# Kernel tuning notes

Measured on AMD Instinct MI355X. Metric: run time of the kernel, lower is better.

Reference implementation:

```python
import jax, jax.numpy as jnp
import numpy as np

CLASS_EMBED_DIM = 128
TOPK = 64
EPS = float(np.finfo(float).eps)
ALPHA = 0.99


def setup_inputs() -> dict:
    key = jax.random.key(0)
    k1, k2, k3 = jax.random.split(key, 3)
    b, n, d = 16, 256, 640  # d = embed_dim + class_embed_dim
    embed_dim, inner_dim = 512, 512
    x = jax.random.normal(k1, (b, n, d), dtype=jnp.float32)
    # kaiming-normal style init: std = sqrt(2 / fan_in)
    std = (2.0 / embed_dim) ** 0.5
    Wq = jax.random.normal(k2, (embed_dim, inner_dim), dtype=jnp.float32) * std
    Wk = jax.random.normal(k3, (embed_dim, inner_dim), dtype=jnp.float32) * std
    alpha = jnp.float32(ALPHA)
    return {"x": x, "Wq": Wq, "Wk": Wk, "alpha": alpha}


def reference(x, Wq, Wk, alpha):
    b, n, d = x.shape
    xf = x.reshape(b * n, d)            # (N, embed+class)
    xe = xf[:, :-CLASS_EMBED_DIM]       # (N, embed)
    q = xe @ Wq                         # (N, inner)
    k = xe @ Wk                         # (N, inner)
    D = q.shape[1]
    # dots[i,j] = mean_d (q_i - k_j)^2, via expansion (avoids N x N x D tensor)
    q2 = jnp.sum(q * q, axis=1)
    k2 = jnp.sum(k * k, axis=1)
    dots = (q2[:, None] + k2[None, :] - 2.0 * (q @ k.T)) / D  # (N, N)
    N = dots.shape[0]
    _, idx = jax.lax.top_k(dots, TOPK)  # largest, matching torch.topk
    mask = jnp.zeros_like(dots).at[jnp.arange(N)[:, None], idx].set(1.0)
    mask = ((mask + mask.T) > 0).astype(jnp.float32)
    attn = dots * mask
    A = jnp.eye(N, dtype=dots.dtype) - alpha * attn + EPS
    out = jnp.linalg.inv(A) @ xf        # (N, d); to_v is identity
    return out.reshape(b, n, d)
```

## Files before the change

kernel.cpp:

```cpp
#include <hip/hip_runtime.h>
#include <float.h>

#define NN 4096
#define DD 640
#define DE 512
#define NB 16
#define OB 128
#define NOB (NN/OB)
#define SB 128
#define NSB (NN/SB)

static __device__ __forceinline__ float4 ldg4(const float* p) { return *(const float4*)p; }

__global__ __launch_bounds__(256) void proj_gemm(
    const float* __restrict__ xf, const float* __restrict__ Wq,
    const float* __restrict__ Wk, float* __restrict__ q, float* __restrict__ kk_)
{
  __shared__ float Xs[32][68], Qs[32][68], Ks[32][68];
  const int i0 = blockIdx.x * 64, c0 = blockIdx.y * 64;
  const int t = threadIdx.x, tr = t >> 4, tc = t & 15;
  float accq[4][4] = {}, acck[4][4] = {};
  for (int kb = 0; kb < DE; kb += 32) {
    {
      int m = t >> 3, k4 = (t & 7) << 2;
      float4 v0 = ldg4(xf + (size_t)(i0 + m) * DD + kb + k4);
      float4 v1 = ldg4(xf + (size_t)(i0 + m + 32) * DD + kb + k4);
      Xs[k4+0][m] = v0.x; Xs[k4+1][m] = v0.y; Xs[k4+2][m] = v0.z; Xs[k4+3][m] = v0.w;
      Xs[k4+0][m+32] = v1.x; Xs[k4+1][m+32] = v1.y; Xs[k4+2][m+32] = v1.z; Xs[k4+3][m+32] = v1.w;
    }
    {
      int kr = t >> 3, n8 = (t & 7) << 3;
      *(float4*)&Qs[kr][n8]   = ldg4(Wq + (size_t)(kb + kr) * DE + c0 + n8);
      *(float4*)&Qs[kr][n8+4] = ldg4(Wq + (size_t)(kb + kr) * DE + c0 + n8 + 4);
      *(float4*)&Ks[kr][n8]   = ldg4(Wk + (size_t)(kb + kr) * DE + c0 + n8);
      *(float4*)&Ks[kr][n8+4] = ldg4(Wk + (size_t)(kb + kr) * DE + c0 + n8 + 4);
    }
    __syncthreads();
    #pragma unroll
    for (int kkk = 0; kkk < 32; ++kkk) {
      float a[4], bq[4], bk[4];
      *(float4*)a  = *(const float4*)&Xs[kkk][tr << 2];
      *(float4*)bq = *(const float4*)&Qs[kkk][tc << 2];
      *(float4*)bk = *(const float4*)&Ks[kkk][tc << 2];
      #pragma unroll
      for (int r = 0; r < 4; ++r)
        #pragma unroll
        for (int c = 0; c < 4; ++c) { accq[r][c] += a[r]*bq[c]; acck[r][c] += a[r]*bk[c]; }
    }
    __syncthreads();
  }
  #pragma unroll
  for (int r = 0; r < 4; ++r) {
    float* qp = q   + (size_t)(i0 + (tr<<2) + r) * DE + c0 + (tc<<2);
    float* kp = kk_ + (size_t)(i0 + (tr<<2) + r) * DE + c0 + (tc<<2);
    *(float4*)qp = make_float4(accq[r][0], accq[r][1], accq[r][2], accq[r][3]);
    *(float4*)kp = make_float4(acck[r][0], acck[r][1], acck[r][2], acck[r][3]);
  }
}

__global__ __launch_bounds__(256) void rownorm(
    const float* __restrict__ q, const float* __restrict__ kk_,
    float* __restrict__ q2, float* __restrict__ k2)
{
  int w = (blockIdx.x * 256 + threadIdx.x) >> 6;
  int lane = threadIdx.x & 63;
  const float* src = (w < NN) ? q : kk_;
  int row = (w < NN) ? w : w - NN;
  const float* p = src + (size_t)row * DE;
  float s = 0.f;
  for (int c = lane; c < DE; c += 64) { float v = p[c]; s += v * v; }
  for (int off = 32; off; off >>= 1) s += __shfl_down(s, off);
  if (lane == 0) { if (w < NN) q2[row] = s; else k2[row] = s; }
}

__global__ __launch_bounds__(256) void dots_gemm128(
    const float* __restrict__ q, const float* __restrict__ kk_,
    const float* __restrict__ q2, const float* __restrict__ k2,
    float* __restrict__ dots)
{
  __shared__ float As[16][132], Bs[16][132];
  const int i0 = blockIdx.x * 128, j0 = blockIdx.y * 128;
  const int t = threadIdx.x;
  const int tr = t >> 4, tc = t & 15;
  float acc[8][8] = {};
  for (int kb = 0; kb < DE; kb += 16) {
    {
      int m = t >> 1, k8 = (t & 1) << 3;
      const float* ap = q + (size_t)(i0 + m) * DE + kb + k8;
      float4 v0 = ldg4(ap), v1 = ldg4(ap + 4);
      As[k8+0][m] = v0.x; As[k8+1][m] = v0.y; As[k8+2][m] = v0.z; As[k8+3][m] = v0.w;
      As[k8+4][m] = v1.x; As[k8+5][m] = v1.y; As[k8+6][m] = v1.z; As[k8+7][m] = v1.w;
      const float* bp = kk_ + (size_t)(j0 + m) * DE + kb + k8;
      float4 w0 = ldg4(bp), w1 = ldg4(bp + 4);
      Bs[k8+0][m] = w0.x; Bs[k8+1][m] = w0.y; Bs[k8+2][m] = w0.z; Bs[k8+3][m] = w0.w;
      Bs[k8+4][m] = w1.x; Bs[k8+5][m] = w1.y; Bs[k8+6][m] = w1.z; Bs[k8+7][m] = w1.w;
    }
    __syncthreads();
    #pragma unroll
    for (int k = 0; k < 16; ++k) {
      float av[8], bv[8];
      *(float4*)av       = *(const float4*)&As[k][tr << 3];
      *(float4*)(av + 4) = *(const float4*)&As[k][(tr << 3) + 4];
      *(float4*)bv       = *(const float4*)&Bs[k][tc << 3];
      *(float4*)(bv + 4) = *(const float4*)&Bs[k][(tc << 3) + 4];
      #pragma unroll
      for (int r = 0; r < 8; ++r)
        #pragma unroll
        for (int c = 0; c < 8; ++c) acc[r][c] += av[r] * bv[c];
    }
    __syncthreads();
  }
  const float inv = 1.0f / (float)DE;
  float k2v[8];
  *(float4*)k2v       = ldg4(k2 + j0 + (tc << 3));
  *(float4*)(k2v + 4) = ldg4(k2 + j0 + (tc << 3) + 4);
  #pragma unroll
  for (int r = 0; r < 8; ++r) {
    float q2v = q2[i0 + (tr << 3) + r];
    float o[8];
    #pragma unroll
    for (int c = 0; c < 8; ++c) o[c] = (q2v + k2v[c] - 2.0f * acc[r][c]) * inv;
    float* dp = dots + (size_t)(i0 + (tr << 3) + r) * NN + j0 + (tc << 3);
    *(float4*)dp       = make_float4(o[0], o[1], o[2], o[3]);
    *(float4*)(dp + 4) = make_float4(o[4], o[5], o[6], o[7]);
  }
}

__global__ __launch_bounds__(256) void topk_bits(
    const float* __restrict__ dots, unsigned int* __restrict__ bits)
{
  __shared__ float row[NN];
  __shared__ unsigned int b[128];
  __shared__ float rv[4]; __shared__ int ri[4];
  const int i = blockIdx.x, t = threadIdx.x;
  const float* dr = dots + (size_t)i * NN;
  for (int c = t; c < NN; c += 256) row[c] = dr[c];
  if (t < 128) b[t] = 0u;
  __syncthreads();
  for (int it = 0; it < 64; ++it) {
    float bv = -FLT_MAX; int bi = NN;
    for (int c = t; c < NN; c += 256) { float v = row[c]; if (v > bv) { bv = v; bi = c; } }
    for (int off = 32; off; off >>= 1) {
      float ov = __shfl_down(bv, off); int oi = __shfl_down(bi, off);
      if (ov > bv || (ov == bv && oi < bi)) { bv = ov; bi = oi; }
    }
    if ((t & 63) == 0) { rv[t >> 6] = bv; ri[t >> 6] = bi; }
    __syncthreads();
    if (t == 0) {
      float fv = rv[0]; int fi = ri[0];
      for (int w = 1; w < 4; ++w)
        if (rv[w] > fv || (rv[w] == fv && ri[w] < fi)) { fv = rv[w]; fi = ri[w]; }
      b[fi >> 5] |= 1u << (fi & 31);
      row[fi] = -FLT_MAX;
    }
    __syncthreads();
  }
  if (t < 128) bits[(size_t)i * 128 + t] = b[t];
}

__global__ __launch_bounds__(256) void build_A(
    float* __restrict__ A, const unsigned int* __restrict__ bits,
    const float* __restrict__ alpha_p)
{
  int tid = blockIdx.x * 256 + threadIdx.x;
  int i = tid >> 10;
  int j4 = (tid & 1023) << 2;
  float alpha = alpha_p[0];
  float* p = A + (size_t)i * NN + j4;
  float4 d = *(float4*)p;
  unsigned int wrow = bits[(size_t)i * 128 + (j4 >> 5)];
  float dv[4] = {d.x, d.y, d.z, d.w}, o[4];
  #pragma unroll
  for (int u = 0; u < 4; ++u) {
    int j = j4 + u;
    unsigned int m1 = (wrow >> (j & 31)) & 1u;
    unsigned int m2 = (bits[(size_t)j * 128 + (i >> 5)] >> (i & 31)) & 1u;
    float base = (i == j) ? 1.0f : 0.0f;
    o[u] = base - ((m1 | m2) ? alpha * dv[u] : 0.0f);
  }
  *(float4*)p = make_float4(o[0], o[1], o[2], o[3]);
}

__global__ __launch_bounds__(256) void pack_panel(
    const float* __restrict__ A, float* __restrict__ P, int ok0)
{
  int r = blockIdx.x * 8 + (threadIdx.x >> 5);
  int c4 = (threadIdx.x & 31) << 2;
  if (r < NN - ok0)
    *(float4*)(P + (size_t)r * OB + c4) = ldg4(A + (size_t)(ok0 + r) * NN + ok0 + c4);
}

__global__ __launch_bounds__(256) void unpack_panel(
    const float* __restrict__ P, float* __restrict__ A, int ok0)
{
  int r = blockIdx.x * 8 + (threadIdx.x >> 5);
  int c4 = (threadIdx.x & 31) << 2;
  if (r < NN - ok0)
    *(float4*)(A + (size_t)(ok0 + r) * NN + ok0 + c4) = ldg4(P + (size_t)r * OB + c4);
}

__global__ __launch_bounds__(1024) void lu_panel(
    float* __restrict__ P, int k0, int ok0, int* __restrict__ piv)
{
  const int t = threadIdx.x;
  const int M = NN - k0;
  const int lk0 = k0 - ok0;
  float a[4][NB];
  __shared__ float rv[2][16]; __shared__ int ri[2][16];
  __shared__ float pb[2][NB];
  __shared__ float bufA[2][NB];
  __shared__ int piv_s[NB];
  __shared__ int sd[32], ss[32];
  __shared__ float l16[16][17];
  __shared__ float gbuf[32][112];

  #pragma unroll
  for (int i = 0; i < 4; ++i) {
    int r = t + (i << 10);
    if (r < M) {
      const float* src = P + (size_t)(lk0 + r) * OB + lk0;
      #pragma unroll
      for (int c4 = 0; c4 < NB; c4 += 4) {
        float4 v = ldg4(src + c4);
        a[i][c4] = v.x; a[i][c4+1] = v.y; a[i][c4+2] = v.z; a[i][c4+3] = v.w;
      }
    }
  }

  #pragma unroll
  for (int j = 0; j < NB; ++j) {
    const int bb = j & 1;
    float bv = -1.0f; int br = 1 << 30;
    #pragma unroll
    for (int i = 0; i < 4; ++i) {
      int r = t + (i << 10);
      if (r >= j && r < M) {
        float v = fabsf(a[i][j]);
        if (v > bv || (v == bv && r < br)) { bv = v; br = r; }
      }
    }
    for (int off = 32; off; off >>= 1) {
      float ov = __shfl_down(bv, off); int orr = __shfl_down(br, off);
      if (ov > bv || (ov == bv && orr < br)) { bv = ov; br = orr; }
    }
    if ((t & 63) == 0) { rv[bb][t >> 6] = bv; ri[bb][t >> 6] = br; }
    __syncthreads();
    float fv = rv[bb][0]; int fr = ri[bb][0];
    #pragma unroll
    for (int w = 1; w < 16; ++w)
      if (rv[bb][w] > fv || (rv[bb][w] == fv && ri[bb][w] < fr)) { fv = rv[bb][w]; fr = ri[bb][w]; }
    const int pr = fr;
    if (t == 0) piv_s[j] = k0 + pr;
    const int prT = pr & 1023, prS = pr >> 10;
    if (t == prT) {
      #pragma unroll
      for (int i2 = 0; i2 < 4; ++i2) if (i2 == prS) {
        #pragma unroll
        for (int c = 0; c < NB; ++c) pb[bb][c] = a[i2][c];
      }
    }
    if (t == j) {
      #pragma unroll
      for (int c = 0; c < NB; ++c) bufA[bb][c] = a[0][c];
    }
    __syncthreads();
    if (t == j) {
      #pragma unroll
      for (int c = 0; c < NB; ++c) a[0][c] = pb[bb][c];
    }
    if (t == prT) {
      #pragma unroll
      for (int i2 = 0; i2 < 4; ++i2) if (i2 == prS) {
        #pragma unroll
        for (int c = 0; c < NB; ++c) a[i2][c] = bufA[bb][c];
      }
    }
    float rp = 1.0f / pb[bb][j];
    #pragma unroll
    for (int i = 0; i < 4; ++i) {
      int r = t + (i << 10);
      if (r > j && r < M) {
        float mlt = a[i][j] * rp;
        a[i][j] = mlt;
        #pragma unroll
        for (int c = j + 1; c < NB; ++c) a[i][c] -= mlt * pb[bb][c];
      }
    }
  }
  __syncthreads();

  #pragma unroll
  for (int i = 0; i < 4; ++i) {
    int r = t + (i << 10);
    if (r < M) {
      float* dst = P + (size_t)(lk0 + r) * OB + lk0;
      #pragma unroll
      for (int c4 = 0; c4 < NB; c4 += 4)
        *(float4*)(dst + c4) = make_float4(a[i][c4], a[i][c4+1], a[i][c4+2], a[i][c4+3]);
    }
  }
  if (t < NB) piv[k0 + t] = piv_s[t];

  if (t < 16) {
    #pragma unroll
    for (int c2 = 0; c2 < NB; ++c2) l16[t][c2] = a[0][c2];
  }

  if (t < 32) {
    int slotrow = (t < NB) ? (k0 + t) : -1;
    int content = slotrow;
    int next_ext = NB;
    for (int j = 0; j < NB; ++j) {
      int p = piv_s[j];
      unsigned long long mask = __ballot(slotrow == p);
      int bslot;
      if (mask) bslot = __ffsll((unsigned long long)mask) - 1;
      else {
        bslot = next_ext;
        if (t == next_ext) { slotrow = p; content = p; }
        next_ext++;
      }
      int srcl = (t == j) ? bslot : ((t == bslot) ? j : t);
      content = __shfl(content, srcl);
    }
    sd[t] = slotrow;
    ss[t] = content;
  }
  __syncthreads();

  const int p16 = lk0;
  for (int idx = t; idx < 32 * 112; idx += 1024) {
    int i = idx / 112, cc = idx - i * 112;
    if (sd[i] >= 0 && sd[i] != ss[i]) {
      int cl = (cc < p16 ? cc : cc + NB);
      gbuf[i][cc] = P[(size_t)(ss[i] - ok0) * OB + cl];
    }
  }
  __syncthreads();
  for (int idx = t; idx < 32 * 112; idx += 1024) {
    int i = idx / 112, cc = idx - i * 112;
    if (sd[i] >= 0 && sd[i] != ss[i]) {
      int cl = (cc < p16 ? cc : cc + NB);
      P[(size_t)(sd[i] - ok0) * OB + cl] = gbuf[i][cc];
    }
  }
  __syncthreads();

  const int w = OB - (lk0 + NB);
  if (t < w) {
    int cl = lk0 + NB + t;
    int cc = p16 + t;
    float x[16];
    #pragma unroll
    for (int i = 0; i < 16; ++i)
      x[i] = (ss[i] != sd[i]) ? gbuf[i][cc] : P[(size_t)(lk0 + i) * OB + cl];
    #pragma unroll
    for (int i = 1; i < 16; ++i)
      #pragma unroll
      for (int j = 0; j < i; ++j) x[i] -= l16[i][j] * x[j];
    #pragma unroll
    for (int i = 0; i < 16; ++i) P[(size_t)(lk0 + i) * OB + cl] = x[i];
  }
}

__global__ __launch_bounds__(64) void net_perm128(
    const int* __restrict__ piv_g, int ok0,
    int* __restrict__ nd, int* __restrict__ ns)
{
  __shared__ int pl[OB];
  const int L = threadIdx.x;
  pl[L] = piv_g[ok0 + L];
  pl[L + 64] = piv_g[ok0 + 64 + L];
  __syncthreads();
  int c0 = ok0 + L, c1 = ok0 + 64 + L, c2 = -1, c3 = -1;
  int sr2 = -1, sr3 = -1;
  int next_ext = 128;
  for (int j = 0; j < OB; ++j) {
    int p = pl[j];
    int s2;
    if (p < ok0 + OB) s2 = p - ok0;
    else {
      unsigned long long m2 = __ballot(sr2 == p);
      unsigned long long m3 = __ballot(sr3 == p);
      if (m2) s2 = 128 + (__ffsll(m2) - 1);
      else if (m3) s2 = 192 + (__ffsll(m3) - 1);
      else {
        s2 = next_ext;
        if (s2 < 192) { if (L == s2 - 128) { sr2 = p; c2 = p; } }
        else          { if (L == s2 - 192) { sr3 = p; c3 = p; } }
        next_ext++;
      }
    }
    int jp = j >> 6, jl = j & 63, sp = s2 >> 6, sl = s2 & 63;
    int vj0 = __shfl(c0, jl), vj1 = __shfl(c1, jl);
    int vj = (jp == 0) ? vj0 : vj1;
    int vs0 = __shfl(c0, sl), vs1 = __shfl(c1, sl), vs2 = __shfl(c2, sl), vs3 = __shfl(c3, sl);
    int vs = (sp == 0) ? vs0 : (sp == 1) ? vs1 : (sp == 2) ? vs2 : vs3;
    if (jp == 0 && L == jl) c0 = vs;
    if (jp == 1 && L == jl) c1 = vs;
    if (sp == 0 && L == sl) c0 = vj;
    if (sp == 1 && L == sl) c1 = vj;
    if (sp == 2 && L == sl) c2 = vj;
    if (sp == 3 && L == sl) c3 = vj;
  }
  nd[L] = ok0 + L;        ns[L] = c0;
  nd[64 + L] = ok0 + 64 + L; ns[64 + L] = c1;
  nd[128 + L] = sr2;      ns[128 + L] = c2;
  nd[192 + L] = sr3;      ns[192 + L] = c3;
}

__global__ __launch_bounds__(256) void perm_copy_out(
    const float* __restrict__ A, float* __restrict__ T,
    const int* __restrict__ nd, const int* __restrict__ ns, int ok0)
{
  int s = blockIdx.y;
  int d = nd[s], sr = ns[s];
  if (d < 0 || d == sr) return;
  int c = blockIdx.x * 1024 + threadIdx.x * 4;
  if (c >= ok0 && c < ok0 + OB) return;
  *(float4*)(T + (size_t)s * NN + c) = ldg4(A + (size_t)sr * NN + c);
}

__global__ __launch_bounds__(256) void perm_copy_in(
    float* __restrict__ A, const float* __restrict__ T,
    const int* __restrict__ nd, const int* __restrict__ ns, int ok0)
{
  int s = blockIdx.y;
  int d = nd[s], sr = ns[s];
  if (d < 0 || d == sr) return;
  int c = blockIdx.x * 1024 + threadIdx.x * 4;
  if (c >= ok0 && c < ok0 + OB) return;
  *(float4*)(A + (size_t)d * NN + c) = ldg4(T + (size_t)s * NN + c);
}

__global__ __launch_bounds__(64) void trsm128L(float* __restrict__ A, int ok0)
{
  __shared__ float Ls[64][65];
  __shared__ float xs[64][133];
  const int t = threadIdx.x;
  const int c = ok0 + OB + blockIdx.x * 64 + t;
  for (int i = 0; i < 128; ++i) xs[t][i] = A[(size_t)(ok0 + i) * NN + c];
  for (int i = 0; i < 64; ++i) Ls[i][t] = A[(size_t)(ok0 + i) * NN + ok0 + t];
  __syncthreads();
  for (int i = 1; i < 64; ++i) {
    float s0 = 0.f, s1 = 0.f, s2 = 0.f, s3 = 0.f;
    int j = 0;
    for (; j + 3 < i; j += 4) {
      s0 += Ls[i][j+0] * xs[t][j+0]; s1 += Ls[i][j+1] * xs[t][j+1];
      s2 += Ls[i][j+2] * xs[t][j+2]; s3 += Ls[i][j+3] * xs[t][j+3];
    }
    for (; j < i; ++j) s0 += Ls[i][j] * xs[t][j];
    xs[t][i] -= (s0 + s1) + (s2 + s3);
  }
  __syncthreads();
  for (int i = 0; i < 64; ++i) Ls[i][t] = A[(size_t)(ok0 + 64 + i) * NN + ok0 + t];
  __syncthreads();
  for (int i = 0; i < 64; ++i) {
    float s0 = 0.f, s1 = 0.f, s2 = 0.f, s3 = 0.f;
    #pragma unroll 4
    for (int j = 0; j < 64; j += 4) {
      s0 += Ls[i][j+0] * xs[t][j+0]; s1 += Ls[i][j+1] * xs[t][j+1];
      s2 += Ls[i][j+2] * xs[t][j+2]; s3 += Ls[i][j+3] * xs[t][j+3];
    }
    xs[t][64 + i] -= (s0 + s1) + (s2 + s3);
  }
  __syncthreads();
  for (int i = 0; i < 64; ++i) Ls[i][t] = A[(size_t)(ok0 + 64 + i) * NN + ok0 + 64 + t];
  __syncthreads();
  for (int i = 1; i < 64; ++i) {
    float s0 = 0.f, s1 = 0.f, s2 = 0.f, s3 = 0.f;
    int j = 0;
    for (; j + 3 < i; j += 4) {
      s0 += Ls[i][j+0] * xs[t][64+j+0]; s1 += Ls[i][j+1] * xs[t][64+j+1];
      s2 += Ls[i][j+2] * xs[t][64+j+2]; s3 += Ls[i][j+3] * xs[t][64+j+3];
    }
    for (; j < i; ++j) s0 += Ls[i][j] * xs[t][64+j];
    xs[t][64 + i] -= (s0 + s1) + (s2 + s3);
  }
  for (int i = 0; i < 128; ++i) A[(size_t)(ok0 + i) * NN + c] = xs[t][i];
}

__global__ __launch_bounds__(256) void rank_update(
    float* __restrict__ C, int ldc,
    const float* __restrict__ Aop, int lda,
    const float* __restrict__ Bop, int ldb,
    int Mr, int Nc, int K)
{
  __shared__ float As[16][68], Bs[16][68];
  const int m0 = blockIdx.x * 64, n0 = blockIdx.y * 64;
  const int t = threadIdx.x, tr = t >> 4, tc = t & 15;
  const float4 z4 = make_float4(0.f, 0.f, 0.f, 0.f);
  float acc[4][4] = {};
  for (int kb = 0; kb < K; kb += 16) {
    {
      int m = t >> 2, k4 = (t & 3) << 2;
      float4 v0 = (m0 + m < Mr) ? ldg4(Aop + (size_t)(m0 + m) * lda + kb + k4) : z4;
      As[k4+0][m] = v0.x; As[k4+1][m] = v0.y; As[k4+2][m] = v0.z; As[k4+3][m] = v0.w;
    }
    {
      int kr = t >> 4, n4 = (t & 15) << 2;
      bool ok = (n0 + n4 < Nc);
      float4 w0 = ok ? ldg4(Bop + (size_t)(kb + kr) * ldb + n0 + n4) : z4;
      *(float4*)&Bs[kr][n4] = w0;
    }
    __syncthreads();
    #pragma unroll
    for (int kkk = 0; kkk < 16; ++kkk) {
      float a[4], b[4];
      *(float4*)a = *(const float4*)&As[kkk][tr << 2];
      *(float4*)b = *(const float4*)&Bs[kkk][tc << 2];
      #pragma unroll
      for (int r = 0; r < 4; ++r)
        #pragma unroll
        for (int c = 0; c < 4; ++c) acc[r][c] += a[r] * b[c];
    }
    __syncthreads();
  }
  #pragma unroll
  for (int r = 0; r < 4; ++r) {
    int m = m0 + (tr << 2) + r;
    int n = n0 + (tc << 2);
    if (m < Mr && n < Nc) {
      float* cp = C + (size_t)m * ldc + n;
      float4 cv = *(float4*)cp;
      cv.x -= acc[r][0]; cv.y -= acc[r][1]; cv.z -= acc[r][2]; cv.w -= acc[r][3];
      *(float4*)cp = cv;
    }
  }
}

__global__ __launch_bounds__(256) void rank_update128(
    float* __restrict__ C, int ldc,
    const float* __restrict__ Aop, int lda,
    const float* __restrict__ Bop, int ldb,
    int K)
{
  __shared__ float As[16][132], Bs[16][132];
  const int m0 = blockIdx.x * 128, n0 = blockIdx.y * 128;
  const int t = threadIdx.x;
  const int tr = t >> 4, tc = t & 15;
  float acc[8][8] = {};
  for (int kb = 0; kb < K; kb += 16) {
    {
      int m = t >> 1, k8 = (t & 1) << 3;
      const float* ap = Aop + (size_t)(m0 + m) * lda + kb + k8;
      float4 v0 = ldg4(ap), v1 = ldg4(ap + 4);
      As[k8+0][m] = v0.x; As[k8+1][m] = v0.y; As[k8+2][m] = v0.z; As[k8+3][m] = v0.w;
      As[k8+4][m] = v1.x; As[k8+5][m] = v1.y; As[k8+6][m] = v1.z; As[k8+7][m] = v1.w;
    }
    {
      int kr = t >> 4, c8 = (t & 15) << 3;
      const float* bp = Bop + (size_t)(kb + kr) * ldb + n0 + c8;
      *(float4*)&Bs[kr][c8]     = ldg4(bp);
      *(float4*)&Bs[kr][c8 + 4] = ldg4(bp + 4);
    }
    __syncthreads();
    #pragma unroll
    for (int k = 0; k < 16; ++k) {
      float av[8], bv[8];
      *(float4*)av       = *(const float4*)&As[k][tr << 3];
      *(float4*)(av + 4) = *(const float4*)&As[k][(tr << 3) + 4];
      *(float4*)bv       = *(const float4*)&Bs[k][tc << 3];
      *(float4*)(bv + 4) = *(const float4*)&Bs[k][(tc << 3) + 4];
      #pragma unroll
      for (int r = 0; r < 8; ++r)
        #pragma unroll
        for (int c = 0; c < 8; ++c) acc[r][c] += av[r] * bv[c];
    }
    __syncthreads();
  }
  #pragma unroll
  for (int r = 0; r < 8; ++r) {
    float* cp = C + (size_t)(m0 + (tr << 3) + r) * ldc + n0 + (tc << 3);
    float4 c0 = *(float4*)cp, c1 = *(float4*)(cp + 4);
    c0.x -= acc[r][0]; c0.y -= acc[r][1]; c0.z -= acc[r][2]; c0.w -= acc[r][3];
    c1.x -= acc[r][4]; c1.y -= acc[r][5]; c1.z -= acc[r][6]; c1.w -= acc[r][7];
    *(float4*)cp = c0; *(float4*)(cp + 4) = c1;
  }
}

__global__ __launch_bounds__(128) void inv_tri(
    const float* __restrict__ Ag, float* __restrict__ invT, int upper)
{
  __shared__ float xs[128][128];
  const int s = blockIdx.x, t = threadIdx.x;
  const size_t r0 = (size_t)s * SB;
  for (int i = 0; i < 128; ++i) xs[i][t] = 0.0f;
  const float* Tb = Ag + r0 * NN + r0;
  if (!upper) {
    xs[t][t] = 1.0f;
    for (int i = 1; i < 128; ++i) {
      float s0 = 0.f, s1 = 0.f, s2 = 0.f, s3 = 0.f;
      int j = 0;
      for (; j + 3 < i; j += 4) {
        s0 += Tb[(size_t)i * NN + j+0] * xs[j+0][t];
        s1 += Tb[(size_t)i * NN + j+1] * xs[j+1][t];
        s2 += Tb[(size_t)i * NN + j+2] * xs[j+2][t];
        s3 += Tb[(size_t)i * NN + j+3] * xs[j+3][t];
      }
      for (; j < i; ++j) s0 += Tb[(size_t)i * NN + j] * xs[j][t];
      float ssum = (s0 + s1) + (s2 + s3);
      if (i != t) xs[i][t] = -ssum;
    }
  } else {
    xs[t][t] = 1.0f / Tb[(size_t)t * NN + t];
    for (int i = 126; i >= 0; --i) {
      float s0 = 0.f, s1 = 0.f, s2 = 0.f, s3 = 0.f;
      int j = i + 1;
      for (; j + 3 < 128; j += 4) {
        s0 += Tb[(size_t)i * NN + j+0] * xs[j+0][t];
        s1 += Tb[(size_t)i * NN + j+1] * xs[j+1][t];
        s2 += Tb[(size_t)i * NN + j+2] * xs[j+2][t];
        s3 += Tb[(size_t)i * NN + j+3] * xs[j+3][t];
      }
      for (; j < 128; ++j) s0 += Tb[(size_t)i * NN + j] * xs[j][t];
      float ssum = (s0 + s1) + (s2 + s3);
      if (i != t) xs[i][t] = -ssum / Tb[(size_t)i * NN + i];
    }
  }
  for (int i = 0; i < 128; ++i) invT[(size_t)s * SB * SB + (size_t)i * SB + t] = xs[i][t];
}

__global__ __launch_bounds__(1024) void perm_compose(
    const int* __restrict__ piv, int* __restrict__ idxp)
{
  __shared__ int pl[NN];
  const int t = threadIdx.x;
  for (int j = t; j < NN; j += 1024) pl[j] = piv[j];
  __syncthreads();
  int pos[4] = { t, t + 1024, t + 2048, t + 3072 };
  for (int j = NN - 1; j >= 0; --j) {
    int p = pl[j];
    #pragma unroll
    for (int u = 0; u < 4; ++u) {
      int r = t + (u << 10);
      if (j <= r) {
        if (pos[u] == j) pos[u] = p;
        else if (pos[u] == p) pos[u] = j;
      }
    }
  }
  #pragma unroll
  for (int u = 0; u < 4; ++u) idxp[t + (u << 10)] = pos[u];
}

__global__ __launch_bounds__(256) void gather_rows(
    const float* __restrict__ xf, const int* __restrict__ idxp, float* __restrict__ out)
{
  const int r = blockIdx.x, t = threadIdx.x;
  const int src = idxp[r];
  const float4* s = (const float4*)(xf + (size_t)src * DD);
  float4* d = (float4*)(out + (size_t)r * DD);
  for (int c = t; c < DD / 4; c += 256) d[c] = s[c];
}

__global__ __launch_bounds__(256) void diag_apply(
    float* __restrict__ B, const float* __restrict__ Minv, int r0)
{
  __shared__ float Bs[128][68];
  const int c0 = blockIdx.x * 64, t = threadIdx.x;
  #pragma unroll
  for (int v = 0; v < 8; ++v) {
    int id = t + v * 256;
    int k = id >> 4, c4 = (id & 15) << 2;
    *(float4*)&Bs[k][c4] = ldg4(B + (size_t)(r0 + k) * DD + c0 + c4);
  }
  __syncthreads();
  const int tr = t >> 4, tc = t & 15;
  float acc[8][4] = {};
  for (int k4 = 0; k4 < 128; k4 += 4) {
    float b0[4], b1[4], b2[4], b3[4];
    *(float4*)b0 = *(const float4*)&Bs[k4+0][tc << 2];
    *(float4*)b1 = *(const float4*)&Bs[k4+1][tc << 2];
    *(float4*)b2 = *(const float4*)&Bs[k4+2][tc << 2];
    *(float4*)b3 = *(const float4*)&Bs[k4+3][tc << 2];
    #pragma unroll
    for (int rr = 0; rr < 8; ++rr) {
      float m[4]; *(float4*)m = ldg4(Minv + (size_t)(tr*8 + rr) * SB + k4);
      #pragma unroll
      for (int c = 0; c < 4; ++c)
        acc[rr][c] += m[0]*b0[c] + m[1]*b1[c] + m[2]*b2[c] + m[3]*b3[c];
    }
  }
  #pragma unroll
  for (int rr = 0; rr < 8; ++rr)
    *(float4*)(B + (size_t)(r0 + tr*8 + rr) * DD + c0 + (tc << 2)) =
        make_float4(acc[rr][0], acc[rr][1], acc[rr][2], acc[rr][3]);
}

extern "C" void kernel_launch(void* const* d_in, const int* in_sizes, int n_in,
                              void* d_out, int out_size, void* d_ws, size_t ws_size,
                              hipStream_t stream)
{
  const float* xf    = (const float*)d_in[0];
  const float* Wq    = (const float*)d_in[1];
  const float* Wk    = (const float*)d_in[2];
  const float* alpha = (const float*)d_in[3];
  float* out = (float*)d_out;
  char* ws = (char*)d_ws;

  float* Amat = (float*)(ws);
  float* q    = (float*)(ws + 67108864ull);
  float* kbuf = (float*)(ws + 75497472ull);
  float* invL = (float*)(ws + 83886080ull);
  float* invU = (float*)(ws + 85983232ull);
  unsigned int* bits = (unsigned int*)(ws + 88080384ull);
  float* q2   = (float*)(ws + 90177536ull);
  float* k2   = (float*)(ws + 90193920ull);
  int* piv    = (int*)(ws + 90210304ull);
  int* idxp   = (int*)(ws + 90226688ull);
  int* nd     = (int*)(ws + 90243072ull);
  int* ns     = (int*)(ws + 90275840ull);
  float* Tbuf = q;
  float* P    = kbuf;

  proj_gemm<<<dim3(NN/64, DE/64), 256, 0, stream>>>(xf, Wq, Wk, q, kbuf);
  rownorm<<<2 * NN / 4, 256, 0, stream>>>(q, kbuf, q2, k2);
  dots_gemm128<<<dim3(NN/128, NN/128), 256, 0, stream>>>(q, kbuf, q2, k2, Amat);
  topk_bits<<<NN, 256, 0, stream>>>(Amat, bits);
  build_A<<<NN * NN / 4 / 256, 256, 0, stream>>>(Amat, bits, alpha);

  for (int ob = 0; ob < NOB; ++ob) {
    const int ok0 = ob * OB;
    const int nrows = NN - ok0;
    pack_panel<<<(nrows + 7) / 8, 256, 0, stream>>>(Amat, P, ok0);
    for (int p = 0; p < OB / NB; ++p) {
      const int k0 = ok0 + p * NB;
      lu_panel<<<1, 1024, 0, stream>>>(P, k0, ok0, piv);
      if (p < OB / NB - 1) {
        const int lk1 = (p + 1) * NB;
        const int w = OB - lk1;
        const int M2 = nrows - lk1;
        rank_update<<<dim3((M2 + 63) / 64, (w + 63) / 64), 256, 0, stream>>>(
            P + (size_t)lk1 * OB + lk1, OB,
            P + (size_t)lk1 * OB + (lk1 - NB), OB,
            P + (size_t)(lk1 - NB) * OB + lk1, OB,
            M2, w, NB);
      }
    }
    unpack_panel<<<(nrows + 7) / 8, 256, 0, stream>>>(P, Amat, ok0);
    net_perm128<<<1, 64, 0, stream>>>(piv, ok0, nd, ns);
    perm_copy_out<<<dim3(NN / 1024, 256), 256, 0, stream>>>(Amat, Tbuf, nd, ns, ok0);
    perm_copy_in<<<dim3(NN / 1024, 256), 256, 0, stream>>>(Amat, Tbuf, nd, ns, ok0);
    const int b1 = ok0 + OB;
    const int M2 = NN - b1;
    if (M2 > 0) {
      trsm128L<<<M2 / 64, 64, 0, stream>>>(Amat, ok0);
      rank_update128<<<dim3(M2 / 128, M2 / 128), 256, 0, stream>>>(
          Amat + (size_t)b1 * NN + b1, NN,
          Amat + (size_t)b1 * NN + ok0, NN,
          Amat + (size_t)ok0 * NN + b1, NN,
          OB);
    }
  }

  inv_tri<<<NSB, 128, 0, stream>>>(Amat, invL, 0);
  inv_tri<<<NSB, 128, 0, stream>>>(Amat, invU, 1);
  perm_compose<<<1, 1024, 0, stream>>>(piv, idxp);
  gather_rows<<<NN, 256, 0, stream>>>(xf, idxp, out);

  for (int s = 0; s < NSB; ++s) {
    int r0 = s * SB;
    diag_apply<<<DD / 64, 256, 0, stream>>>(out, invL + (size_t)s * SB * SB, r0);
    if (r0 + SB < NN) {
      int M2 = NN - r0 - SB;
      rank_update128<<<dim3(M2 / 128, DD / 128), 256, 0, stream>>>(
          out + (size_t)(r0 + SB) * DD, DD,
          Amat + (size_t)(r0 + SB) * NN + r0, NN,
          out + (size_t)r0 * DD, DD,
          SB);
    }
  }
  for (int s = NSB - 1; s >= 0; --s) {
    int r0 = s * SB;
    diag_apply<<<DD / 64, 256, 0, stream>>>(out, invU + (size_t)s * SB * SB, r0);
    if (r0 > 0) {
      rank_update128<<<dim3(r0 / 128, DD / 128), 256, 0, stream>>>(
          out, DD,
          Amat + r0, NN,
          out + (size_t)r0 * DD, DD,
          SB);
    }
  }
}
```

Before: 39.65 ms.

## Fuse panel LU and rank updates into one cooperative kernel with grid sync

Replaces the per-16-column sequence of lu_panel and rank_update launches with a single cooperative kernel per 128-wide block column. Workgroup 0 factors each sub-panel and the whole grid of 120 workgroups then does the trailing update, with grid.sync between phases. The goal is to remove about 15 kernel launches per outer block and the gaps between them. In exchange the factoring block drops from 1024 to 512 threads with more registers per thread, and each step pays for grid-wide barriers.

```diff
diff --git a/kernel.cpp b/kernel.cpp
--- a/kernel.cpp
+++ b/kernel.cpp
@@ -1,5 +1,8 @@
 #include <hip/hip_runtime.h>
+#include <hip/hip_cooperative_groups.h>
 #include <float.h>
+
+namespace cg = cooperative_groups;
 
 #define NN 4096
 #define DD 640
@@ -9,6 +12,7 @@
 #define NOB (NN/OB)
 #define SB 128
 #define NSB (NN/SB)
+#define LU_NWG 120
 
 static __device__ __forceinline__ float4 ldg4(const float* p) { return *(const float4*)p; }
 
@@ -199,167 +203,230 @@
     *(float4*)(A + (size_t)(ok0 + r) * NN + ok0 + c4) = ldg4(P + (size_t)r * OB + c4);
 }
 
-__global__ __launch_bounds__(1024) void lu_panel(
-    float* __restrict__ P, int k0, int ok0, int* __restrict__ piv)
-{
+__global__ __launch_bounds__(512) void lu_block_coop(
+    float* __restrict__ P, int ok0, int* __restrict__ piv)
+{
+  cg::grid_group grid = cg::this_grid();
   const int t = threadIdx.x;
-  const int M = NN - k0;
-  const int lk0 = k0 - ok0;
-  float a[4][NB];
-  __shared__ float rv[2][16]; __shared__ int ri[2][16];
+  const int wg = blockIdx.x;
+  const int nwg = gridDim.x;
+  const int nrows = NN - ok0;
+
+  __shared__ float rv[2][8]; __shared__ int ri[2][8];
   __shared__ float pb[2][NB];
   __shared__ float bufA[2][NB];
   __shared__ int piv_s[NB];
   __shared__ int sd[32], ss[32];
   __shared__ float l16[16][17];
   __shared__ float gbuf[32][112];
-
-  #pragma unroll
-  for (int i = 0; i < 4; ++i) {
-    int r = t + (i << 10);
-    if (r < M) {
-      const float* src = P + (size_t)(lk0 + r) * OB + lk0;
+  __shared__ float As[16][68], Bs[16][68];
+
+  for (int p = 0; p < OB / NB; ++p) {
+    const int k0 = ok0 + p * NB;
+    const int lk0 = p * NB;
+    const int M = NN - k0;
+
+    if (wg == 0) {
+      float a[8][NB];
       #pragma unroll
-      for (int c4 = 0; c4 < NB; c4 += 4) {
-        float4 v = ldg4(src + c4);
-        a[i][c4] = v.x; a[i][c4+1] = v.y; a[i][c4+2] = v.z; a[i][c4+3] = v.w;
-      }
-    }
-  }
-
-  #pragma unroll
-  for (int j = 0; j < NB; ++j) {
-    const int bb = j & 1;
-    float bv = -1.0f; int br = 1 << 30;
-    #pragma unroll
-    for (int i = 0; i < 4; ++i) {
-      int r = t + (i << 10);
-      if (r >= j && r < M) {
-        float v = fabsf(a[i][j]);
-        if (v > bv || (v == bv && r < br)) { bv = v; br = r; }
-      }
-    }
-    for (int off = 32; off; off >>= 1) {
-      float ov = __shfl_down(bv, off); int orr = __shfl_down(br, off);
-      if (ov > bv || (ov == bv && orr < br)) { bv = ov; br = orr; }
-    }
-    if ((t & 63) == 0) { rv[bb][t >> 6] = bv; ri[bb][t >> 6] = br; }
-    __syncthreads();
-    float fv = rv[bb][0]; int fr = ri[bb][0];
-    #pragma unroll
-    for (int w = 1; w < 16; ++w)
-      if (rv[bb][w] > fv || (rv[bb][w] == fv && ri[bb][w] < fr)) { fv = rv[bb][w]; fr = ri[bb][w]; }
-    const int pr = fr;
-    if (t == 0) piv_s[j] = k0 + pr;
-    const int prT = pr & 1023, prS = pr >> 10;
-    if (t == prT) {
+      for (int i = 0; i < 8; ++i) {
+        int r = t + (i << 9);
+        if (r < M) {
+          const float* src = P + (size_t)(lk0 + r) * OB + lk0;
+          #pragma unroll
+          for (int c4 = 0; c4 < NB; c4 += 4) {
+            float4 v = ldg4(src + c4);
+            a[i][c4] = v.x; a[i][c4+1] = v.y; a[i][c4+2] = v.z; a[i][c4+3] = v.w;
+          }
+        }
+      }
       #pragma unroll
-      for (int i2 = 0; i2 < 4; ++i2) if (i2 == prS) {
-        #pragma unroll
-        for (int c = 0; c < NB; ++c) pb[bb][c] = a[i2][c];
-      }
-    }
-    if (t == j) {
+      for (int j = 0; j < NB; ++j) {
+        const int bb = j & 1;
+        float bv = -1.0f; int br = 1 << 30;
+        #pragma unroll
+        for (int i = 0; i < 8; ++i) {
+          int r = t + (i << 9);
+          if (r >= j && r < M) {
+            float v = fabsf(a[i][j]);
+            if (v > bv || (v == bv && r < br)) { bv = v; br = r; }
+          }
+        }
+        for (int off = 32; off; off >>= 1) {
+          float ov = __shfl_down(bv, off); int orr = __shfl_down(br, off);
+          if (ov > bv || (ov == bv && orr < br)) { bv = ov; br = orr; }
+        }
+        if ((t & 63) == 0) { rv[bb][t >> 6] = bv; ri[bb][t >> 6] = br; }
+        __syncthreads();
+        float fv = rv[bb][0]; int fr = ri[bb][0];
+        #pragma unroll
+        for (int w = 1; w < 8; ++w)
+          if (rv[bb][w] > fv || (rv[bb][w] == fv && ri[bb][w] < fr)) { fv = rv[bb][w]; fr = ri[bb][w]; }
+        const int pr = fr;
+        if (t == 0) piv_s[j] = k0 + pr;
+        const int prT = pr & 511, prS = pr >> 9;
+        if (t == prT) {
+          #pragma unroll
+          for (int i2 = 0; i2 < 8; ++i2) if (i2 == prS) {
+            #pragma unroll
+            for (int c = 0; c < NB; ++c) pb[bb][c] = a[i2][c];
+          }
+        }
+        if (t == j) {
+          #pragma unroll
+          for (int c = 0; c < NB; ++c) bufA[bb][c] = a[0][c];
+        }
+        __syncthreads();
+        if (t == j) {
+          #pragma unroll
+          for (int c = 0; c < NB; ++c) a[0][c] = pb[bb][c];
+        }
+        if (t == prT) {
+          #pragma unroll
+          for (int i2 = 0; i2 < 8; ++i2) if (i2 == prS) {
+            #pragma unroll
+            for (int c = 0; c < NB; ++c) a[i2][c] = bufA[bb][c];
+          }
+        }
+        float rp = 1.0f / pb[bb][j];
+        #pragma unroll
+        for (int i = 0; i < 8; ++i) {
+          int r = t + (i << 9);
+          if (r > j && r < M) {
+            float mlt = a[i][j] * rp;
+            a[i][j] = mlt;
+            #pragma unroll
+            for (int c = j + 1; c < NB; ++c) a[i][c] -= mlt * pb[bb][c];
+          }
+        }
+      }
+      __syncthreads();
+
       #pragma unroll
-      for (int c = 0; c < NB; ++c) bufA[bb][c] = a[0][c];
-    }
-    __syncthreads();
-    if (t == j) {
-      #pragma unroll
-      for (int c = 0; c < NB; ++c) a[0][c] = pb[bb][c];
-    }
-    if (t == prT) {
-      #pragma unroll
-      for (int i2 = 0; i2 < 4; ++i2) if (i2 == prS) {
-        #pragma unroll
-        for (int c = 0; c < NB; ++c) a[i2][c] = bufA[bb][c];
-      }
-    }
-    float rp = 1.0f / pb[bb][j];
-    #pragma unroll
-    for (int i = 0; i < 4; ++i) {
-      int r = t + (i << 10);
-      if (r > j && r < M) {
-        float mlt = a[i][j] * rp;
-        a[i][j] = mlt;
-        #pragma unroll
-        for (int c = j + 1; c < NB; ++c) a[i][c] -= mlt * pb[bb][c];
-      }
-    }
-  }
-  __syncthreads();
-
-  #pragma unroll
-  for (int i = 0; i < 4; ++i) {
-    int r = t + (i << 10);
-    if (r < M) {
-      float* dst = P + (size_t)(lk0 + r) * OB + lk0;
-      #pragma unroll
-      for (int c4 = 0; c4 < NB; c4 += 4)
-        *(float4*)(dst + c4) = make_float4(a[i][c4], a[i][c4+1], a[i][c4+2], a[i][c4+3]);
-    }
-  }
-  if (t < NB) piv[k0 + t] = piv_s[t];
-
-  if (t < 16) {
-    #pragma unroll
-    for (int c2 = 0; c2 < NB; ++c2) l16[t][c2] = a[0][c2];
-  }
-
-  if (t < 32) {
-    int slotrow = (t < NB) ? (k0 + t) : -1;
-    int content = slotrow;
-    int next_ext = NB;
-    for (int j = 0; j < NB; ++j) {
-      int p = piv_s[j];
-      unsigned long long mask = __ballot(slotrow == p);
-      int bslot;
-      if (mask) bslot = __ffsll((unsigned long long)mask) - 1;
-      else {
-        bslot = next_ext;
-        if (t == next_ext) { slotrow = p; content = p; }
-        next_ext++;
-      }
-      int srcl = (t == j) ? bslot : ((t == bslot) ? j : t);
-      content = __shfl(content, srcl);
-    }
-    sd[t] = slotrow;
-    ss[t] = content;
-  }
-  __syncthreads();
-
-  const int p16 = lk0;
-  for (int idx = t; idx < 32 * 112; idx += 1024) {
-    int i = idx / 112, cc = idx - i * 112;
-    if (sd[i] >= 0 && sd[i] != ss[i]) {
-      int cl = (cc < p16 ? cc : cc + NB);
-      gbuf[i][cc] = P[(size_t)(ss[i] - ok0) * OB + cl];
-    }
-  }
-  __syncthreads();
-  for (int idx = t; idx < 32 * 112; idx += 1024) {
-    int i = idx / 112, cc = idx - i * 112;
-    if (sd[i] >= 0 && sd[i] != ss[i]) {
-      int cl = (cc < p16 ? cc : cc + NB);
-      P[(size_t)(sd[i] - ok0) * OB + cl] = gbuf[i][cc];
-    }
-  }
-  __syncthreads();
-
-  const int w = OB - (lk0 + NB);
-  if (t < w) {
-    int cl = lk0 + NB + t;
-    int cc = p16 + t;
-    float x[16];
-    #pragma unroll
-    for (int i = 0; i < 16; ++i)
-      x[i] = (ss[i] != sd[i]) ? gbuf[i][cc] : P[(size_t)(lk0 + i) * OB + cl];
-    #pragma unroll
-    for (int i = 1; i < 16; ++i)
-      #pragma unroll
-      for (int j = 0; j < i; ++j) x[i] -= l16[i][j] * x[j];
-    #pragma unroll
-    for (int i = 0; i < 16; ++i) P[(size_t)(lk0 + i) * OB + cl] = x[i];
+      for (int i = 0; i < 8; ++i) {
+        int r = t + (i << 9);
+        if (r < M) {
+          float* dst = P + (size_t)(lk0 + r) * OB + lk0;
+          #pragma unroll
+          for (int c4 = 0; c4 < NB; c4 += 4)
+            *(float4*)(dst + c4) = make_float4(a[i][c4], a[i][c4+1], a[i][c4+2], a[i][c4+3]);
+        }
+      }
+      if (t < NB) piv[k0 + t] = piv_s[t];
+
+      if (t < 16) {
+        #pragma unroll
+        for (int c2 = 0; c2 < NB; ++c2) l16[t][c2] = a[0][c2];
+      }
+
+      if (t < 32) {
+        int slotrow = (t < NB) ? (k0 + t) : -1;
+        int content = slotrow;
+        int next_ext = NB;
+        for (int j = 0; j < NB; ++j) {
+          int pp = piv_s[j];
+          unsigned long long mask = __ballot(slotrow == pp);
+          int bslot;
+          if (mask) bslot = __ffsll((unsigned long long)mask) - 1;
+          else {
+            bslot = next_ext;
+            if (t == next_ext) { slotrow = pp; content = pp; }
+            next_ext++;
+          }
+          int srcl = (t == j) ? bslot : ((t == bslot) ? j : t);
+          content = __shfl(content, srcl);
+        }
+        sd[t] = slotrow;
+        ss[t] = content;
+      }
+      __syncthreads();
+
+      const int p16 = lk0;
+      for (int idx = t; idx < 32 * 112; idx += 512) {
+        int i = idx / 112, cc = idx - i * 112;
+        if (sd[i] >= 0 && sd[i] != ss[i]) {
+          int cl = (cc < p16 ? cc : cc + NB);
+          gbuf[i][cc] = P[(size_t)(ss[i] - ok0) * OB + cl];
+        }
+      }
+      __syncthreads();
+      for (int idx = t; idx < 32 * 112; idx += 512) {
+        int i = idx / 112, cc = idx - i * 112;
+        if (sd[i] >= 0 && sd[i] != ss[i]) {
+          int cl = (cc < p16 ? cc : cc + NB);
+          P[(size_t)(sd[i] - ok0) * OB + cl] = gbuf[i][cc];
+        }
+      }
+      __syncthreads();
+
+      const int w = OB - (lk0 + NB);
+      if (t < w) {
+        int cl = lk0 + NB + t;
+        int cc = p16 + t;
+        float x[16];
+        #pragma unroll
+        for (int i = 0; i < 16; ++i)
+          x[i] = (ss[i] != sd[i]) ? gbuf[i][cc] : P[(size_t)(lk0 + i) * OB + cl];
+        #pragma unroll
+        for (int i = 1; i < 16; ++i)
+          #pragma unroll
+          for (int j = 0; j < i; ++j) x[i] -= l16[i][j] * x[j];
+        #pragma unroll
+        for (int i = 0; i < 16; ++i) P[(size_t)(lk0 + i) * OB + cl] = x[i];
+      }
+    }
+    grid.sync();
+
+    if (p < OB / NB - 1) {
+      const int lk1 = lk0 + NB;
+      const int w = OB - lk1;
+      const int M2 = nrows - lk1;
+      float* C = P + (size_t)lk1 * OB + lk1;
+      const float* Ao = P + (size_t)lk1 * OB + lk0;
+      const float* Bo = P + (size_t)lk0 * OB + lk1;
+      const int tm = (M2 + 63) >> 6, tn = (w + 63) >> 6;
+      const float4 z4 = make_float4(0.f, 0.f, 0.f, 0.f);
+      for (int tile = wg; tile < tm * tn; tile += nwg) {
+        const int m0 = (tile / tn) << 6, n0 = (tile % tn) << 6;
+        float acc[4][4] = {};
+        if (t < 256) {
+          int m = t >> 2, k4 = (t & 3) << 2;
+          float4 v0 = (m0 + m < M2) ? ldg4(Ao + (size_t)(m0 + m) * OB + k4) : z4;
+          As[k4+0][m] = v0.x; As[k4+1][m] = v0.y; As[k4+2][m] = v0.z; As[k4+3][m] = v0.w;
+          int kr = t >> 4, n4 = (t & 15) << 2;
+          bool ok = (n0 + n4 < w);
+          float4 w0 = ok ? ldg4(Bo + (size_t)kr * OB + n0 + n4) : z4;
+          *(float4*)&Bs[kr][n4] = w0;
+        }
+        __syncthreads();
+        if (t < 256) {
+          const int tr = t >> 4, tc = t & 15;
+          #pragma unroll
+          for (int kkk = 0; kkk < 16; ++kkk) {
+            float a[4], b[4];
+            *(float4*)a = *(const float4*)&As[kkk][tr << 2];
+            *(float4*)b = *(const float4*)&Bs[kkk][tc << 2];
+            #pragma unroll
+            for (int r = 0; r < 4; ++r)
+              #pragma unroll
+              for (int c = 0; c < 4; ++c) acc[r][c] += a[r] * b[c];
+          }
+          #pragma unroll
+          for (int r = 0; r < 4; ++r) {
+            int m = m0 + (tr << 2) + r;
+            int n = n0 + (tc << 2);
+            if (m < M2 && n < w) {
+              float* cp = C + (size_t)m * OB + n;
+              float4 cv = *(float4*)cp;
+              cv.x -= acc[r][0]; cv.y -= acc[r][1]; cv.z -= acc[r][2]; cv.w -= acc[r][3];
+              *(float4*)cp = cv;
+            }
+          }
+        }
+        __syncthreads();
+      }
+      grid.sync();
+    }
   }
 }
 
@@ -480,55 +547,6 @@
   for (int i = 0; i < 128; ++i) A[(size_t)(ok0 + i) * NN + c] = xs[t][i];
 }
 
-__global__ __launch_bounds__(256) void rank_update(
-    float* __restrict__ C, int ldc,
-    const float* __restrict__ Aop, int lda,
-    const float* __restrict__ Bop, int ldb,
-    int Mr, int Nc, int K)
-{
-  __shared__ float As[16][68], Bs[16][68];
-  const int m0 = blockIdx.x * 64, n0 = blockIdx.y * 64;
-  const int t = threadIdx.x, tr = t >> 4, tc = t & 15;
-  const float4 z4 = make_float4(0.f, 0.f, 0.f, 0.f);
-  float acc[4][4] = {};
-  for (int kb = 0; kb < K; kb += 16) {
-    {
-      int m = t >> 2, k4 = (t & 3) << 2;
-      float4 v0 = (m0 + m < Mr) ? ldg4(Aop + (size_t)(m0 + m) * lda + kb + k4) : z4;
-      As[k4+0][m] = v0.x; As[k4+1][m] = v0.y; As[k4+2][m] = v0.z; As[k4+3][m] = v0.w;
-    }
-    {
-      int kr = t >> 4, n4 = (t & 15) << 2;
-      bool ok = (n0 + n4 < Nc);
-      float4 w0 = ok ? ldg4(Bop + (size_t)(kb + kr) * ldb + n0 + n4) : z4;
-      *(float4*)&Bs[kr][n4] = w0;
-    }
-    __syncthreads();
-    #pragma unroll
-    for (int kkk = 0; kkk < 16; ++kkk) {
-      float a[4], b[4];
-      *(float4*)a = *(const float4*)&As[kkk][tr << 2];
-      *(float4*)b = *(const float4*)&Bs[kkk][tc << 2];
-      #pragma unroll
-      for (int r = 0; r < 4; ++r)
-        #pragma unroll
-        for (int c = 0; c < 4; ++c) acc[r][c] += a[r] * b[c];
-    }
-    __syncthreads();
-  }
-  #pragma unroll
-  for (int r = 0; r < 4; ++r) {
-    int m = m0 + (tr << 2) + r;
-    int n = n0 + (tc << 2);
-    if (m < Mr && n < Nc) {
-      float* cp = C + (size_t)m * ldc + n;
-      float4 cv = *(float4*)cp;
-      cv.x -= acc[r][0]; cv.y -= acc[r][1]; cv.z -= acc[r][2]; cv.w -= acc[r][3];
-      *(float4*)cp = cv;
-    }
-  }
-}
-
 __global__ __launch_bounds__(256) void rank_update128(
     float* __restrict__ C, int ldc,
     const float* __restrict__ Aop, int lda,
@@ -724,19 +742,11 @@
     const int ok0 = ob * OB;
     const int nrows = NN - ok0;
     pack_panel<<<(nrows + 7) / 8, 256, 0, stream>>>(Amat, P, ok0);
-    for (int p = 0; p < OB / NB; ++p) {
-      const int k0 = ok0 + p * NB;
-      lu_panel<<<1, 1024, 0, stream>>>(P, k0, ok0, piv);
-      if (p < OB / NB - 1) {
-        const int lk1 = (p + 1) * NB;
-        const int w = OB - lk1;
-        const int M2 = nrows - lk1;
-        rank_update<<<dim3((M2 + 63) / 64, (w + 63) / 64), 256, 0, stream>>>(
-            P + (size_t)lk1 * OB + lk1, OB,
-            P + (size_t)lk1 * OB + (lk1 - NB), OB,
-            P + (size_t)(lk1 - NB) * OB + lk1, OB,
-            M2, w, NB);
-      }
+    {
+      float* Pp = P; int ok0v = ok0; int* pivp = piv;
+      void* kargs[] = { (void*)&Pp, (void*)&ok0v, (void*)&pivp };
+      hipLaunchCooperativeKernel((void*)lu_block_coop, dim3(LU_NWG), dim3(512),
+                                 kargs, 0, stream);
     }
     unpack_panel<<<(nrows + 7) / 8, 256, 0, stream>>>(P, Amat, ok0);
     net_perm128<<<1, 64, 0, stream>>>(piv, ok0, nd, ns);
```

Result: slower. 49.72 ms (+25.4%).
